# Kernel optimization log

Hardware: AMD Instinct MI355X
Metric: run time of the kernel (lower is better)

## Reference

```python
import jax, jax.numpy as jnp
import numpy as np
import math

B, T, HIDDEN = 1, 2048, 2048
N_HEADS, N_KV = 16, 8
HD = HIDDEN // N_HEADS  # 128
EPS = 1e-6
THETA = 1e6


def _rmsnorm(x, w, eps=EPS):
    return x * jax.lax.rsqrt(jnp.mean(x * x, axis=-1, keepdims=True) + eps) * w


def _rope(x, sin, cos):
    # even/odd split, non-interleaved concat output (matches get_rope)
    x1 = x[..., 0::2]
    x2 = x[..., 1::2]
    s = sin[None, :, None, :]  # [1, T, 1, HD//2]
    c = cos[None, :, None, :]
    return jnp.concatenate([x1 * c - x2 * s, x1 * s + x2 * c], axis=-1)


def setup_inputs() -> dict:
    key = jax.random.key(0)
    ks = jax.random.split(key, 6)
    x = jax.random.normal(ks[0], (B, T, HIDDEN), dtype=jnp.float32)
    Wq = 0.02 * jax.random.normal(ks[1], (HIDDEN, 2 * HIDDEN), dtype=jnp.float32)
    Wk = 0.02 * jax.random.normal(ks[2], (HIDDEN, N_KV * HD), dtype=jnp.float32)
    Wv = 0.02 * jax.random.normal(ks[3], (HIDDEN, N_KV * HD), dtype=jnp.float32)
    Wo = 0.02 * jax.random.normal(ks[4], (2 * HIDDEN, HIDDEN), dtype=jnp.float32)
    q_norm_w = jnp.ones((2 * HD,), dtype=jnp.float32)
    k_norm_w = jnp.ones((HD,), dtype=jnp.float32)
    inv_freq = 1.0 / (THETA ** (jnp.arange(0, HD, 2, dtype=jnp.float32) / HD))
    freqs = jnp.arange(T, dtype=jnp.float32)[:, None] * inv_freq[None, :]  # [T, HD//2]
    return {"x": x, "Wq": Wq, "Wk": Wk, "Wv": Wv, "Wo": Wo,
            "q_norm_w": q_norm_w, "k_norm_w": k_norm_w,
            "sin": jnp.sin(freqs), "cos": jnp.cos(freqs)}


def reference(x, Wq, Wk, Wv, Wo, q_norm_w, k_norm_w, sin, cos):
    b, t, _ = x.shape
    # projections
    q = (x @ Wq).reshape(b, t, N_HEADS, 2 * HD)
    k = (x @ Wk).reshape(b, t, N_KV, HD)
    v = (x @ Wv).reshape(b, t, N_KV, HD)
    # per-head QK RMSNorm (q_norm over 2*head_dim)
    q = _rmsnorm(q, q_norm_w)
    k = _rmsnorm(k, k_norm_w)
    # split q into 2*N_HEADS attention heads of dim HD, apply RoPE
    hq = 2 * N_HEADS
    q = _rope(q.reshape(b, t, hq, HD), sin, cos)
    k = _rope(k, sin, cos)
    # GQA: repeat kv heads
    g = hq // N_KV
    k = jnp.repeat(k, g, axis=2)  # [b, t, hq, HD]
    v = jnp.repeat(v, g, axis=2)
    # attention: no causal mask in the original module
    att = jnp.einsum('bqhd,bkhd->bhqk', q, k) / math.sqrt(HD)
    p = jax.nn.softmax(att, axis=-1)
    out = jnp.einsum('bhqk,bkhd->bqhd', p, v).reshape(b, t, hq * HD)
    return out @ Wo
```

## Files before the change

### kernel.cpp

```cpp
#include <hip/hip_runtime.h>

typedef unsigned short u16;
typedef __attribute__((ext_vector_type(8))) short bf16x8;
typedef __attribute__((ext_vector_type(4))) short s16x4;
typedef __attribute__((ext_vector_type(4))) float f32x4;

__device__ __forceinline__ float bf2f(u16 u) {
  union { unsigned u; float f; } c; c.u = ((unsigned)u) << 16; return c.f;
}
__device__ __forceinline__ u16 f2bf(float f) {
  union { float f; unsigned u; } c; c.f = f;
  return (u16)((c.u + 0x7fffu + ((c.u >> 16) & 1u)) >> 16);
}
#if __has_builtin(__builtin_amdgcn_cvt_pk_bf16_f32)
__device__ __forceinline__ unsigned pkbf(float a, float b) {
  auto v = __builtin_amdgcn_cvt_pk_bf16_f32(a, b);
  return __builtin_bit_cast(unsigned, v);
}
#else
__device__ __forceinline__ unsigned pkbf(float a, float b) {
  return (unsigned)f2bf(a) | ((unsigned)f2bf(b) << 16);
}
#endif
#if __has_builtin(__builtin_amdgcn_mfma_f32_16x16x16bf16_1k)
#define MFMA16(a, b, c) __builtin_amdgcn_mfma_f32_16x16x16bf16_1k(a, b, c, 0, 0, 0)
#define HAVE_MFMA16 1
#endif
#if __has_builtin(__builtin_amdgcn_permlane16_swap) && \
    __has_builtin(__builtin_amdgcn_permlane32_swap)
#define HAVE_PLSWAP 1
__device__ __forceinline__ void plswap32(unsigned& a, unsigned& b) {
  auto r = __builtin_amdgcn_permlane32_swap(a, b, false, false);
  a = r[0]; b = r[1];
}
__device__ __forceinline__ void plswap16(unsigned& a, unsigned& b) {
  auto r = __builtin_amdgcn_permlane16_swap(a, b, false, false);
  a = r[0]; b = r[1];
}
#endif
#if __has_builtin(__builtin_amdgcn_exp2f)
#define EXP2(x) __builtin_amdgcn_exp2f(x)
#else
#define EXP2(x) __expf((x) * 0.69314718f)
#endif
__device__ __forceinline__ void gl2lds16(const u16* g, u16* l) {
  __builtin_amdgcn_global_load_lds(
      (const __attribute__((address_space(1))) void*)g,
      (__attribute__((address_space(3))) void*)l, 16, 0, 0);
}

__device__ __forceinline__ void tr_cast_tile(const float* __restrict__ in,
                                             u16* __restrict__ out,
                                             int ldin, int ldout, int bx, int by) {
  __shared__ u16 tile[64][66];
  const int tx = threadIdx.x;
  const int lr = tx & 31, lc = tx >> 5;
  const int r0 = by << 6, c0 = bx << 6;
#pragma unroll
  for (int i = 0; i < 8; ++i) {
    int r = lc + (i << 3);
    float2 v = *(const float2*)&in[(size_t)(r0 + r) * ldin + c0 + (lr << 1)];
    *(unsigned*)&tile[r][lr << 1] = pkbf(v.x, v.y);
  }
  __syncthreads();
#pragma unroll
  for (int i = 0; i < 8; ++i) {
    int c = lc + (i << 3);
    unsigned v = (unsigned)tile[lr << 1][c] | ((unsigned)tile[(lr << 1) + 1][c] << 16);
    *(unsigned*)&out[(size_t)(c0 + c) * ldout + r0 + (lr << 1)] = v;
  }
}

__global__ __launch_bounds__(256) void prep(const float* __restrict__ x,
                                            u16* __restrict__ xb,
                                            const float* __restrict__ Wq,
                                            u16* __restrict__ WqT,
                                            const float* __restrict__ Wk,
                                            u16* __restrict__ WkT,
                                            const float* __restrict__ Wv,
                                            u16* __restrict__ WvT) {
  int b = blockIdx.x;
  if (b < 2048) {
    int i = (b * 256 + threadIdx.x) * 8;
    float4 a = *(const float4*)&x[i];
    float4 c = *(const float4*)&x[i + 4];
    union { unsigned u[4]; bf16x8 v; } w;
    w.u[0] = pkbf(a.x, a.y); w.u[1] = pkbf(a.z, a.w);
    w.u[2] = pkbf(c.x, c.y); w.u[3] = pkbf(c.z, c.w);
    *(bf16x8*)&xb[i] = w.v;
  } else if (b < 4096) {
    int t = b - 2048;
    tr_cast_tile(Wq, WqT, 4096, 2048, t & 63, t >> 6);
  } else if (b < 4608) {
    int t = b - 4096;
    tr_cast_tile(Wk, WkT, 1024, 2048, t & 15, t >> 4);
  } else {
    int t = b - 4608;
    tr_cast_tile(Wv, WvT, 1024, 2048, t & 15, t >> 4);
  }
}

__global__ __launch_bounds__(256) void transpose_cast(const float* __restrict__ in,
                                                      u16* __restrict__ out,
                                                      int ldin, int ldout) {
  tr_cast_tile(in, out, ldin, ldout, blockIdx.x, blockIdx.y);
}

__global__ __launch_bounds__(256) void gemm_bt(const u16* __restrict__ A,
                                               const u16* __restrict__ BT,
                                               u16* __restrict__ C,
                                               int M, int N, int K) {
  __shared__ u16 Asl[2][128 * 32];
  __shared__ u16 Bsl[2][128 * 32];
  const int tid = threadIdx.x;
  const int lane = tid & 63, wv = tid >> 6;
  const int lr = lane & 15, qd = lane >> 4;
  const int wr = wv >> 1, wc = wv & 1;
  const int m0 = blockIdx.y << 7, n0 = blockIdx.x << 7;
  const int srow = lane >> 2, scol = (lane & 3) << 3;
  const u16* Ag = &A[(size_t)(m0 + wv * 32 + srow) * K + scol];
  const u16* Bg = &BT[(size_t)(n0 + wv * 32 + srow) * K + scol];
  const size_t rstr16 = (size_t)16 * K;
  f32x4 acc[4][4] = {};
  for (int k0 = 0; k0 < K; k0 += 64) {
    __syncthreads();
#pragma unroll
    for (int p = 0; p < 2; ++p) {
#pragma unroll
      for (int hh = 0; hh < 2; ++hh) {
        gl2lds16(Ag + k0 + p * 32 + hh * rstr16, &Asl[p][wv * 1024 + hh * 512]);
        gl2lds16(Bg + k0 + p * 32 + hh * rstr16, &Bsl[p][wv * 1024 + hh * 512]);
      }
    }
    __syncthreads();
#pragma unroll
    for (int p = 0; p < 2; ++p) {
      bf16x8 af[4], bfr[4];
#pragma unroll
      for (int i = 0; i < 4; ++i) {
        af[i]  = *(const bf16x8*)&Asl[p][(wr * 64 + i * 16 + lr) * 32 + qd * 8];
        bfr[i] = *(const bf16x8*)&Bsl[p][(wc * 64 + i * 16 + lr) * 32 + qd * 8];
      }
#pragma unroll
      for (int mi = 0; mi < 4; ++mi)
#pragma unroll
        for (int ni = 0; ni < 4; ++ni)
          acc[mi][ni] = __builtin_amdgcn_mfma_f32_16x16x32_bf16(
              af[mi], bfr[ni], acc[mi][ni], 0, 0, 0);
    }
  }
#pragma unroll
  for (int mi = 0; mi < 4; ++mi)
#pragma unroll
    for (int ni = 0; ni < 4; ++ni)
#pragma unroll
      for (int r = 0; r < 4; ++r)
        C[(size_t)(m0 + wr * 64 + mi * 16 + qd * 4 + r) * N +
          n0 + wc * 64 + ni * 16 + lr] = f2bf(acc[mi][ni][r]);
}

__global__ __launch_bounds__(256) void gemm_bt_sk(const u16* __restrict__ A,
                                                  const u16* __restrict__ BT,
                                                  float* __restrict__ C,
                                                  int M, int N, int K, int kspan) {
  __shared__ u16 Asl[2][128 * 32];
  __shared__ u16 Bsl[2][128 * 32];
  const int tid = threadIdx.x;
  const int lane = tid & 63, wv = tid >> 6;
  const int lr = lane & 15, qd = lane >> 4;
  const int wr = wv >> 1, wc = wv & 1;
  const int m0 = blockIdx.y << 7, n0 = blockIdx.x << 7;
  const int kbeg = blockIdx.z * kspan;
  const int srow = lane >> 2, scol = (lane & 3) << 3;
  const u16* Ag = &A[(size_t)(m0 + wv * 32 + srow) * K + kbeg + scol];
  const u16* Bg = &BT[(size_t)(n0 + wv * 32 + srow) * K + kbeg + scol];
  const size_t rstr16 = (size_t)16 * K;
  f32x4 acc[4][4] = {};
  for (int k0 = 0; k0 < kspan; k0 += 64) {
    __syncthreads();
#pragma unroll
    for (int p = 0; p < 2; ++p) {
#pragma unroll
      for (int hh = 0; hh < 2; ++hh) {
        gl2lds16(Ag + k0 + p * 32 + hh * rstr16, &Asl[p][wv * 1024 + hh * 512]);
        gl2lds16(Bg + k0 + p * 32 + hh * rstr16, &Bsl[p][wv * 1024 + hh * 512]);
      }
    }
    __syncthreads();
#pragma unroll
    for (int p = 0; p < 2; ++p) {
      bf16x8 af[4], bfr[4];
#pragma unroll
      for (int i = 0; i < 4; ++i) {
        af[i]  = *(const bf16x8*)&Asl[p][(wr * 64 + i * 16 + lr) * 32 + qd * 8];
        bfr[i] = *(const bf16x8*)&Bsl[p][(wc * 64 + i * 16 + lr) * 32 + qd * 8];
      }
#pragma unroll
      for (int mi = 0; mi < 4; ++mi)
#pragma unroll
        for (int ni = 0; ni < 4; ++ni)
          acc[mi][ni] = __builtin_amdgcn_mfma_f32_16x16x32_bf16(
              af[mi], bfr[ni], acc[mi][ni], 0, 0, 0);
    }
  }
#pragma unroll
  for (int mi = 0; mi < 4; ++mi)
#pragma unroll
    for (int ni = 0; ni < 4; ++ni)
#pragma unroll
      for (int r = 0; r < 4; ++r)
        unsafeAtomicAdd(&C[(size_t)(m0 + wr * 64 + mi * 16 + qd * 4 + r) * N +
                           n0 + wc * 64 + ni * 16 + lr], acc[mi][ni][r]);
}

__global__ __launch_bounds__(256) void norm_vt(u16* __restrict__ QKV,
                                               u16* __restrict__ VTb,
                                               const float* __restrict__ qw,
                                               const float* __restrict__ kw,
                                               const float* __restrict__ sinb,
                                               const float* __restrict__ cosb) {
  int b = blockIdx.x;
  if (b >= 2048) {
    __shared__ u16 tile[64][66];
    int t = b - 2048;
    const int tx = threadIdx.x;
    const int lr = tx & 31, lc = tx >> 5;
    const int r0 = (t >> 4) << 6, c0 = (t & 15) << 6;
    const u16* in = QKV + 5120;
#pragma unroll
    for (int i = 0; i < 8; ++i) {
      int r = lc + (i << 3);
      unsigned v = *(const unsigned*)&in[(size_t)(r0 + r) * 6144 + c0 + (lr << 1)];
      *(unsigned*)&tile[r][lr << 1] = v;
    }
    __syncthreads();
#pragma unroll
    for (int i = 0; i < 8; ++i) {
      int c = lc + (i << 3);
      unsigned v = (unsigned)tile[lr << 1][c] | ((unsigned)tile[(lr << 1) + 1][c] << 16);
      *(unsigned*)&VTb[(size_t)(c0 + c) * 2048 + r0 + (lr << 1)] = v;
    }
    return;
  }
  const int t = b;
  const int wv = threadIdx.x >> 6, l = threadIdx.x & 63;
  const float sv = sinb[t * 64 + l];
  const float cv = cosb[t * 64 + l];
  const float qscale = 0.12753102543f;
  u16* Q = QKV + (size_t)t * 6144;
  u16* Kb = Q + 4096;
  for (int j = wv; j < 16; j += 4) {
    u16* base = Q + j * 256;
    float x0 = bf2f(base[2 * l]);
    float x1 = bf2f(base[2 * l + 1]);
    float x2 = bf2f(base[128 + 2 * l]);
    float x3 = bf2f(base[129 + 2 * l]);
    float ss = x0 * x0 + x1 * x1 + x2 * x2 + x3 * x3;
#pragma unroll
    for (int m = 1; m < 64; m <<= 1) ss += __shfl_xor(ss, m, 64);
    float rn = rsqrtf(ss * (1.0f / 256.0f) + 1e-6f);
    float w0 = qw[2 * l], w1 = qw[2 * l + 1];
    float w2 = qw[128 + 2 * l], w3 = qw[129 + 2 * l];
    x0 *= rn * w0; x1 *= rn * w1; x2 *= rn * w2; x3 *= rn * w3;
    base[l]       = f2bf((x0 * cv - x1 * sv) * qscale);
    base[64 + l]  = f2bf((x0 * sv + x1 * cv) * qscale);
    base[128 + l] = f2bf((x2 * cv - x3 * sv) * qscale);
    base[192 + l] = f2bf((x2 * sv + x3 * cv) * qscale);
  }
  for (int j = wv; j < 8; j += 4) {
    u16* base = Kb + j * 128;
    float x0 = bf2f(base[2 * l]);
    float x1 = bf2f(base[2 * l + 1]);
    float ss = x0 * x0 + x1 * x1;
#pragma unroll
    for (int m = 1; m < 64; m <<= 1) ss += __shfl_xor(ss, m, 64);
    float rn = rsqrtf(ss * (1.0f / 128.0f) + 1e-6f);
    float w0 = kw[2 * l], w1 = kw[2 * l + 1];
    x0 *= rn * w0; x1 *= rn * w1;
    base[l]      = f2bf(x0 * cv - x1 * sv);
    base[64 + l] = f2bf(x0 * sv + x1 * cv);
  }
}

__global__ __launch_bounds__(256, 2) void flash(const u16* __restrict__ QKV,
                                                const u16* __restrict__ VTb,
                                                u16* __restrict__ O0,
                                                u16* __restrict__ O1,
                                                float* __restrict__ L0,
                                                float* __restrict__ L1) {
  __shared__ u16 Ks0[64 * 128];
  __shared__ u16 Ks1[64 * 128];
  __shared__ u16 Vs0[128 * 64];
  __shared__ u16 Vs1[128 * 64];
  const int tid = threadIdx.x;
  const int wv = tid >> 6, lane = tid & 63;
  const int c = lane & 15, qd = lane >> 4;
  const int h = blockIdx.y, kv = h >> 2;
  const int qb = (blockIdx.x << 7) + wv * 32;
  const int z = blockIdx.z;
  u16* Ob = z ? O1 : O0;
  float* Lb = z ? L1 : L0;
  const int cx = c & 7;
  const int krow_off = lane >> 4;
  const int kpb = lane & 15;
  const int vrow_off = lane >> 3;
  const int vpb = lane & 7;
  bf16x8 qf[2][4];
#pragma unroll
  for (int ms = 0; ms < 2; ++ms)
#pragma unroll
    for (int ks = 0; ks < 4; ++ks)
      qf[ms][ks] = *(const bf16x8*)&QKV[(size_t)(qb + ms * 16 + c) * 6144 +
                                        h * 128 + ks * 32 + qd * 8];
  f32x4 o[2][8] = {};
  float lrun[2] = {0.f, 0.f};

  auto stage = [&](int k0, u16* Kd, u16* Vd) {
#pragma unroll
    for (int it = 0; it < 4; ++it) {
      int rbase = (wv * 4 + it) * 4;
      int r = rbase + krow_off;
      int klb = kpb ^ (r & 7);
      gl2lds16(&QKV[(size_t)(k0 + r) * 6144 + 4096 + kv * 128 + klb * 8],
               &Kd[rbase * 128]);
      int dbase = (wv * 4 + it) * 8;
      int d = dbase + vrow_off;
      int vlb = vpb ^ (d & 7);
      gl2lds16(&VTb[(size_t)(kv * 128 + d) * 2048 + k0 + vlb * 8],
               &Vd[dbase * 64]);
    }
  };

  auto compute = [&](const u16* Ks, const u16* Vs) {
    f32x4 s[2][4];
    __builtin_amdgcn_s_setprio(1);
#pragma unroll
    for (int ns = 0; ns < 4; ++ns) {
      f32x4 a0 = {0.f, 0.f, 0.f, 0.f}, a1 = {0.f, 0.f, 0.f, 0.f};
#pragma unroll
      for (int ks = 0; ks < 4; ++ks) {
        bf16x8 kf = *(const bf16x8*)
            &Ks[(ns * 16 + c) * 128 + (((4 * ks + qd) ^ cx) << 3)];
        a0 = __builtin_amdgcn_mfma_f32_16x16x32_bf16(kf, qf[0][ks], a0, 0, 0, 0);
        a1 = __builtin_amdgcn_mfma_f32_16x16x32_bf16(kf, qf[1][ks], a1, 0, 0, 0);
      }
      s[0][ns] = a0; s[1][ns] = a1;
    }
    __builtin_amdgcn_s_setprio(0);
#pragma unroll
    for (int ms = 0; ms < 2; ++ms) {
      float rs = 0.f;
#pragma unroll
      for (int ns = 0; ns < 4; ++ns)
#pragma unroll
        for (int r = 0; r < 4; ++r) {
          float p = EXP2(s[ms][ns][r]);
          s[ms][ns][r] = p; rs += p;
        }
      lrun[ms] += rs;
    }
#ifdef HAVE_PLSWAP
#pragma unroll
    for (int t2 = 0; t2 < 2; ++t2) {
      bf16x8 pB[2];
#pragma unroll
      for (int ms = 0; ms < 2; ++ms) {
        unsigned p0 = pkbf(s[ms][2 * t2][0],     s[ms][2 * t2][1]);
        unsigned p1 = pkbf(s[ms][2 * t2][2],     s[ms][2 * t2][3]);
        unsigned p2 = pkbf(s[ms][2 * t2 + 1][0], s[ms][2 * t2 + 1][1]);
        unsigned p3 = pkbf(s[ms][2 * t2 + 1][2], s[ms][2 * t2 + 1][3]);
        plswap32(p0, p2); plswap16(p0, p2);
        plswap32(p1, p3); plswap16(p1, p3);
        union { unsigned u[4]; bf16x8 v; } bb;
        bb.u[0] = p0; bb.u[1] = p1; bb.u[2] = p2; bb.u[3] = p3;
        pB[ms] = bb.v;
      }
      __builtin_amdgcn_s_setprio(1);
#pragma unroll
      for (int n8 = 0; n8 < 8; ++n8) {
        bf16x8 vf = *(const bf16x8*)
            &Vs[(n8 * 16 + c) * 64 + (((4 * t2 + qd) ^ cx) << 3)];
        o[0][n8] = __builtin_amdgcn_mfma_f32_16x16x32_bf16(vf, pB[0], o[0][n8], 0, 0, 0);
        o[1][n8] = __builtin_amdgcn_mfma_f32_16x16x32_bf16(vf, pB[1], o[1][n8], 0, 0, 0);
      }
      __builtin_amdgcn_s_setprio(0);
    }
#elif defined(HAVE_MFMA16)
#pragma unroll
    for (int ns = 0; ns < 4; ++ns) {
      s16x4 pb[2];
#pragma unroll
      for (int ms = 0; ms < 2; ++ms) {
        union { unsigned u[2]; s16x4 v; } pu;
        pu.u[0] = pkbf(s[ms][ns][0], s[ms][ns][1]);
        pu.u[1] = pkbf(s[ms][ns][2], s[ms][ns][3]);
        pb[ms] = pu.v;
      }
      const int voff = ((((2 * ns) + (qd >> 1)) ^ cx) << 3) + (qd & 1) * 4;
#pragma unroll
      for (int n8 = 0; n8 < 8; ++n8) {
        s16x4 vf = *(const s16x4*)&Vs[(n8 * 16 + c) * 64 + voff];
        o[0][n8] = MFMA16(vf, pb[0], o[0][n8]);
        o[1][n8] = MFMA16(vf, pb[1], o[1][n8]);
      }
    }
#else
    unsigned pk[2][4][2];
#pragma unroll
    for (int ms = 0; ms < 2; ++ms)
#pragma unroll
      for (int ns = 0; ns < 4; ++ns) {
        pk[ms][ns][0] = pkbf(s[ms][ns][0], s[ms][ns][1]);
        pk[ms][ns][1] = pkbf(s[ms][ns][2], s[ms][ns][3]);
      }
    const bool hi = lane >= 32;
    const int sl0 = ((lane >> 4) & 1) * 32 + c;
    const int sl1 = sl0 + 16;
#pragma unroll
    for (int t2 = 0; t2 < 2; ++t2) {
      union { int i[4]; bf16x8 v; } pb[2];
#pragma unroll
      for (int ms = 0; ms < 2; ++ms)
#pragma unroll
        for (int dw = 0; dw < 4; ++dw) {
          int rg = dw & 1;
          int sl = dw < 2 ? sl0 : sl1;
          int va = __shfl((int)pk[ms][2 * t2][rg], sl, 64);
          int vb = __shfl((int)pk[ms][2 * t2 + 1][rg], sl, 64);
          pb[ms].i[dw] = hi ? vb : va;
        }
#pragma unroll
      for (int n8 = 0; n8 < 8; ++n8) {
        bf16x8 vf = *(const bf16x8*)
            &Vs[(n8 * 16 + c) * 64 + (((4 * t2 + qd) ^ cx) << 3)];
        o[0][n8] = __builtin_amdgcn_mfma_f32_16x16x32_bf16(vf, pb[0].v, o[0][n8], 0, 0, 0);
        o[1][n8] = __builtin_amdgcn_mfma_f32_16x16x32_bf16(vf, pb[1].v, o[1][n8], 0, 0, 0);
      }
    }
#endif
  };

  const int kbeg = z << 10, kend = kbeg + 1024;
  stage(kbeg, Ks0, Vs0);
#pragma unroll 1
  for (int k0 = kbeg; k0 < kend; k0 += 128) {
    __syncthreads();
    stage(k0 + 64, Ks1, Vs1);
    compute(Ks0, Vs0);
    __syncthreads();
    if (k0 + 128 < kend) stage(k0 + 128, Ks0, Vs0);
    compute(Ks1, Vs1);
  }
#pragma unroll
  for (int ms = 0; ms < 2; ++ms) {
    lrun[ms] += __shfl_xor(lrun[ms], 16, 64);
    lrun[ms] += __shfl_xor(lrun[ms], 32, 64);
  }
  if (qd == 0) {
    Lb[(qb + c) * 32 + h] = lrun[0];
    Lb[(qb + 16 + c) * 32 + h] = lrun[1];
  }
#pragma unroll
  for (int ms = 0; ms < 2; ++ms)
#pragma unroll
    for (int n8 = 0; n8 < 8; ++n8) {
      union { unsigned u[2]; s16x4 v; } w;
      w.u[0] = pkbf(o[ms][n8][0], o[ms][n8][1]);
      w.u[1] = pkbf(o[ms][n8][2], o[ms][n8][3]);
      *(s16x4*)&Ob[(size_t)(qb + ms * 16 + c) * 4096 + h * 128 + n8 * 16 + qd * 4] = w.v;
    }
}

__global__ __launch_bounds__(256) void combine(u16* __restrict__ O0,
                                               const u16* __restrict__ O1,
                                               const float* __restrict__ L0,
                                               const float* __restrict__ L1) {
  int i8 = (blockIdx.x * 256 + threadIdx.x) * 8;
  int q = i8 >> 12, h = (i8 >> 7) & 31;
  float inv = 1.0f / (L0[q * 32 + h] + L1[q * 32 + h]);
  bf16x8 a = *(bf16x8*)&O0[i8];
  bf16x8 b = *(const bf16x8*)&O1[i8];
  union { unsigned u[4]; bf16x8 v; } w;
#pragma unroll
  for (int j = 0; j < 4; ++j) {
    float e0 = (bf2f((u16)a[2 * j]) + bf2f((u16)b[2 * j])) * inv;
    float e1 = (bf2f((u16)a[2 * j + 1]) + bf2f((u16)b[2 * j + 1])) * inv;
    w.u[j] = pkbf(e0, e1);
  }
  *(bf16x8*)&O0[i8] = w.v;
}

extern "C" void kernel_launch(void* const* d_in, const int* in_sizes, int n_in,
                              void* d_out, int out_size, void* d_ws, size_t ws_size,
                              hipStream_t stream) {
  const float* x    = (const float*)d_in[0];
  const float* Wq   = (const float*)d_in[1];
  const float* Wk   = (const float*)d_in[2];
  const float* Wv   = (const float*)d_in[3];
  const float* Wo   = (const float*)d_in[4];
  const float* qnw  = (const float*)d_in[5];
  const float* knw  = (const float*)d_in[6];
  const float* sinb = (const float*)d_in[7];
  const float* cosb = (const float*)d_in[8];
  float* out = (float*)d_out;
  char* ws = (char*)d_ws;
  const size_t MB = 1024 * 1024;
  u16* WqkvT = (u16*)(ws + 0 * MB);
  u16* Op0   = (u16*)(ws + 0 * MB);
  float* L0f = (float*)(ws + 16 * MB);
  float* L1f = (float*)(ws + 16 * MB + 262144);
  u16* QKV = (u16*)(ws + 24 * MB);
  u16* WoT = (u16*)(ws + 24 * MB);
  u16* xb  = (u16*)(ws + 48 * MB);
  u16* Op1 = (u16*)(ws + 48 * MB);
  u16* VTb = (u16*)(ws + 64 * MB);

  prep<<<5120, 256, 0, stream>>>(x, xb, Wq, WqkvT,
                                 Wk, WqkvT + (size_t)4096 * 2048,
                                 Wv, WqkvT + (size_t)5120 * 2048);
  gemm_bt<<<dim3(48, 16), 256, 0, stream>>>(xb, WqkvT, QKV, 2048, 6144, 2048);
  norm_vt<<<2560, 256, 0, stream>>>(QKV, VTb, qnw, knw, sinb, cosb);
  flash<<<dim3(16, 32, 2), 256, 0, stream>>>(QKV, VTb, Op0, Op1, L0f, L1f);
  transpose_cast<<<dim3(32, 64), 256, 0, stream>>>(Wo, WoT, 2048, 4096);
  combine<<<4096, 256, 0, stream>>>(Op0, Op1, L0f, L1f);
  hipMemsetAsync(out, 0, (size_t)2048 * 2048 * 4, stream);
  gemm_bt_sk<<<dim3(16, 16, 2), 256, 0, stream>>>(Op0, WoT, out, 2048, 2048, 4096, 2048);
  (void)in_sizes; (void)n_in; (void)out_size; (void)ws_size;
}
```

Baseline: 383.4 us.

## Enlarge flash query tile to 64 rows per wave and remap grid by KV group

Each wave now processes 64 query rows instead of 32, so every K/V fragment read from LDS feeds four MFMAs rather than two, and the block covers 256 queries. The grid becomes 1D with 512 blocks, ordered so consecutive blocks share a KV head and key-split half, which is meant to improve L2 reuse of K/V. The compute loop is restructured to interleave QK and PV per 32-key half to limit live score registers. The cost is much higher register pressure (o accumulators double to 128 floats) under launch_bounds(256,2), which risks spills or lower occupancy, and half as many blocks are launched.

New measurement: 733.7 us. 1.91x slower.

```diff
diff --git a/kernel.cpp b/kernel.cpp
--- a/kernel.cpp
+++ b/kernel.cpp
@@ -295,9 +295,11 @@
   const int tid = threadIdx.x;
   const int wv = tid >> 6, lane = tid & 63;
   const int c = lane & 15, qd = lane >> 4;
-  const int h = blockIdx.y, kv = h >> 2;
-  const int qb = (blockIdx.x << 7) + wv * 32;
-  const int z = blockIdx.z;
+  const int s_ = blockIdx.x;
+  const int g = s_ & 15, i_ = s_ >> 4;
+  const int kv = g >> 1, z = g & 1;
+  const int h = kv * 4 + (i_ >> 3);
+  const int qb = ((i_ & 7) << 8) + wv * 64;
   u16* Ob = z ? O1 : O0;
   float* Lb = z ? L1 : L0;
   const int cx = c & 7;
@@ -305,15 +307,15 @@
   const int kpb = lane & 15;
   const int vrow_off = lane >> 3;
   const int vpb = lane & 7;
-  bf16x8 qf[2][4];
-#pragma unroll
-  for (int ms = 0; ms < 2; ++ms)
+  bf16x8 qf[4][4];
+#pragma unroll
+  for (int ms = 0; ms < 4; ++ms)
 #pragma unroll
     for (int ks = 0; ks < 4; ++ks)
       qf[ms][ks] = *(const bf16x8*)&QKV[(size_t)(qb + ms * 16 + c) * 6144 +
                                         h * 128 + ks * 32 + qd * 8];
-  f32x4 o[2][8] = {};
-  float lrun[2] = {0.f, 0.f};
+  f32x4 o[4][8] = {};
+  float lrun[4] = {0.f, 0.f, 0.f, 0.f};
 
   auto stage = [&](int k0, u16* Kd, u16* Vd) {
 #pragma unroll
@@ -332,43 +334,49 @@
   };
 
   auto compute = [&](const u16* Ks, const u16* Vs) {
-    f32x4 s[2][4];
-    __builtin_amdgcn_s_setprio(1);
-#pragma unroll
-    for (int ns = 0; ns < 4; ++ns) {
-      f32x4 a0 = {0.f, 0.f, 0.f, 0.f}, a1 = {0.f, 0.f, 0.f, 0.f};
-#pragma unroll
-      for (int ks = 0; ks < 4; ++ks) {
-        bf16x8 kf = *(const bf16x8*)
-            &Ks[(ns * 16 + c) * 128 + (((4 * ks + qd) ^ cx) << 3)];
-        a0 = __builtin_amdgcn_mfma_f32_16x16x32_bf16(kf, qf[0][ks], a0, 0, 0, 0);
-        a1 = __builtin_amdgcn_mfma_f32_16x16x32_bf16(kf, qf[1][ks], a1, 0, 0, 0);
-      }
-      s[0][ns] = a0; s[1][ns] = a1;
-    }
-    __builtin_amdgcn_s_setprio(0);
-#pragma unroll
-    for (int ms = 0; ms < 2; ++ms) {
-      float rs = 0.f;
-#pragma unroll
-      for (int ns = 0; ns < 4; ++ns)
-#pragma unroll
-        for (int r = 0; r < 4; ++r) {
-          float p = EXP2(s[ms][ns][r]);
-          s[ms][ns][r] = p; rs += p;
+#pragma unroll
+    for (int t2 = 0; t2 < 2; ++t2) {
+      f32x4 s[4][2];
+      __builtin_amdgcn_s_setprio(1);
+#pragma unroll
+      for (int j = 0; j < 2; ++j) {
+        int ns = 2 * t2 + j;
+        f32x4 a[4];
+#pragma unroll
+        for (int ms = 0; ms < 4; ++ms) a[ms] = f32x4{0.f, 0.f, 0.f, 0.f};
+#pragma unroll
+        for (int ks = 0; ks < 4; ++ks) {
+          bf16x8 kf = *(const bf16x8*)
+              &Ks[(ns * 16 + c) * 128 + (((4 * ks + qd) ^ cx) << 3)];
+#pragma unroll
+          for (int ms = 0; ms < 4; ++ms)
+            a[ms] = __builtin_amdgcn_mfma_f32_16x16x32_bf16(kf, qf[ms][ks],
+                                                            a[ms], 0, 0, 0);
         }
-      lrun[ms] += rs;
-    }
+#pragma unroll
+        for (int ms = 0; ms < 4; ++ms) s[ms][j] = a[ms];
+      }
+      __builtin_amdgcn_s_setprio(0);
+#pragma unroll
+      for (int ms = 0; ms < 4; ++ms) {
+        float rs = 0.f;
+#pragma unroll
+        for (int j = 0; j < 2; ++j)
+#pragma unroll
+          for (int r = 0; r < 4; ++r) {
+            float p = EXP2(s[ms][j][r]);
+            s[ms][j][r] = p; rs += p;
+          }
+        lrun[ms] += rs;
+      }
 #ifdef HAVE_PLSWAP
-#pragma unroll
-    for (int t2 = 0; t2 < 2; ++t2) {
-      bf16x8 pB[2];
-#pragma unroll
-      for (int ms = 0; ms < 2; ++ms) {
-        unsigned p0 = pkbf(s[ms][2 * t2][0],     s[ms][2 * t2][1]);
-        unsigned p1 = pkbf(s[ms][2 * t2][2],     s[ms][2 * t2][3]);
-        unsigned p2 = pkbf(s[ms][2 * t2 + 1][0], s[ms][2 * t2 + 1][1]);
-        unsigned p3 = pkbf(s[ms][2 * t2 + 1][2], s[ms][2 * t2 + 1][3]);
+      bf16x8 pB[4];
+#pragma unroll
+      for (int ms = 0; ms < 4; ++ms) {
+        unsigned p0 = pkbf(s[ms][0][0], s[ms][0][1]);
+        unsigned p1 = pkbf(s[ms][0][2], s[ms][0][3]);
+        unsigned p2 = pkbf(s[ms][1][0], s[ms][1][1]);
+        unsigned p3 = pkbf(s[ms][1][2], s[ms][1][3]);
         plswap32(p0, p2); plswap16(p0, p2);
         plswap32(p1, p3); plswap16(p1, p3);
         union { unsigned u[4]; bf16x8 v; } bb;
@@ -380,64 +388,35 @@
       for (int n8 = 0; n8 < 8; ++n8) {
         bf16x8 vf = *(const bf16x8*)
             &Vs[(n8 * 16 + c) * 64 + (((4 * t2 + qd) ^ cx) << 3)];
-        o[0][n8] = __builtin_amdgcn_mfma_f32_16x16x32_bf16(vf, pB[0], o[0][n8], 0, 0, 0);
-        o[1][n8] = __builtin_amdgcn_mfma_f32_16x16x32_bf16(vf, pB[1], o[1][n8], 0, 0, 0);
+#pragma unroll
+        for (int ms = 0; ms < 4; ++ms)
+          o[ms][n8] = __builtin_amdgcn_mfma_f32_16x16x32_bf16(vf, pB[ms],
+                                                              o[ms][n8], 0, 0, 0);
       }
       __builtin_amdgcn_s_setprio(0);
-    }
 #elif defined(HAVE_MFMA16)
 #pragma unroll
-    for (int ns = 0; ns < 4; ++ns) {
-      s16x4 pb[2];
-#pragma unroll
-      for (int ms = 0; ms < 2; ++ms) {
-        union { unsigned u[2]; s16x4 v; } pu;
-        pu.u[0] = pkbf(s[ms][ns][0], s[ms][ns][1]);
-        pu.u[1] = pkbf(s[ms][ns][2], s[ms][ns][3]);
-        pb[ms] = pu.v;
-      }
-      const int voff = ((((2 * ns) + (qd >> 1)) ^ cx) << 3) + (qd & 1) * 4;
-#pragma unroll
-      for (int n8 = 0; n8 < 8; ++n8) {
-        s16x4 vf = *(const s16x4*)&Vs[(n8 * 16 + c) * 64 + voff];
-        o[0][n8] = MFMA16(vf, pb[0], o[0][n8]);
-        o[1][n8] = MFMA16(vf, pb[1], o[1][n8]);
-      }
-    }
-#else
-    unsigned pk[2][4][2];
-#pragma unroll
-    for (int ms = 0; ms < 2; ++ms)
-#pragma unroll
-      for (int ns = 0; ns < 4; ++ns) {
-        pk[ms][ns][0] = pkbf(s[ms][ns][0], s[ms][ns][1]);
-        pk[ms][ns][1] = pkbf(s[ms][ns][2], s[ms][ns][3]);
-      }
-    const bool hi = lane >= 32;
-    const int sl0 = ((lane >> 4) & 1) * 32 + c;
-    const int sl1 = sl0 + 16;
-#pragma unroll
-    for (int t2 = 0; t2 < 2; ++t2) {
-      union { int i[4]; bf16x8 v; } pb[2];
-#pragma unroll
-      for (int ms = 0; ms < 2; ++ms)
-#pragma unroll
-        for (int dw = 0; dw < 4; ++dw) {
-          int rg = dw & 1;
-          int sl = dw < 2 ? sl0 : sl1;
-          int va = __shfl((int)pk[ms][2 * t2][rg], sl, 64);
-          int vb = __shfl((int)pk[ms][2 * t2 + 1][rg], sl, 64);
-          pb[ms].i[dw] = hi ? vb : va;
+      for (int j = 0; j < 2; ++j) {
+        int ns = 2 * t2 + j;
+        s16x4 pb[4];
+#pragma unroll
+        for (int ms = 0; ms < 4; ++ms) {
+          union { unsigned u[2]; s16x4 v; } pu;
+          pu.u[0] = pkbf(s[ms][j][0], s[ms][j][1]);
+          pu.u[1] = pkbf(s[ms][j][2], s[ms][j][3]);
+          pb[ms] = pu.v;
         }
-#pragma unroll
-      for (int n8 = 0; n8 < 8; ++n8) {
-        bf16x8 vf = *(const bf16x8*)
-            &Vs[(n8 * 16 + c) * 64 + (((4 * t2 + qd) ^ cx) << 3)];
-        o[0][n8] = __builtin_amdgcn_mfma_f32_16x16x32_bf16(vf, pb[0].v, o[0][n8], 0, 0, 0);
-        o[1][n8] = __builtin_amdgcn_mfma_f32_16x16x32_bf16(vf, pb[1].v, o[1][n8], 0, 0, 0);
-      }
-    }
+        const int voff = ((((2 * ns) + (qd >> 1)) ^ cx) << 3) + (qd & 1) * 4;
+#pragma unroll
+        for (int n8 = 0; n8 < 8; ++n8) {
+          s16x4 vf = *(const s16x4*)&Vs[(n8 * 16 + c) * 64 + voff];
+#pragma unroll
+          for (int ms = 0; ms < 4; ++ms)
+            o[ms][n8] = MFMA16(vf, pb[ms], o[ms][n8]);
+        }
+      }
 #endif
+    }
   };
 
   const int kbeg = z << 10, kend = kbeg + 1024;
@@ -452,16 +431,17 @@
     compute(Ks1, Vs1);
   }
 #pragma unroll
-  for (int ms = 0; ms < 2; ++ms) {
+  for (int ms = 0; ms < 4; ++ms) {
     lrun[ms] += __shfl_xor(lrun[ms], 16, 64);
     lrun[ms] += __shfl_xor(lrun[ms], 32, 64);
   }
   if (qd == 0) {
-    Lb[(qb + c) * 32 + h] = lrun[0];
-    Lb[(qb + 16 + c) * 32 + h] = lrun[1];
-  }
-#pragma unroll
-  for (int ms = 0; ms < 2; ++ms)
+#pragma unroll
+    for (int ms = 0; ms < 4; ++ms)
+      Lb[(qb + ms * 16 + c) * 32 + h] = lrun[ms];
+  }
+#pragma unroll
+  for (int ms = 0; ms < 4; ++ms)
 #pragma unroll
     for (int n8 = 0; n8 < 8; ++n8) {
       union { unsigned u[2]; s16x4 v; } w;
@@ -520,7 +500,7 @@
                                  Wv, WqkvT + (size_t)5120 * 2048);
   gemm_bt<<<dim3(48, 16), 256, 0, stream>>>(xb, WqkvT, QKV, 2048, 6144, 2048);
   norm_vt<<<2560, 256, 0, stream>>>(QKV, VTb, qnw, knw, sinb, cosb);
-  flash<<<dim3(16, 32, 2), 256, 0, stream>>>(QKV, VTb, Op0, Op1, L0f, L1f);
+  flash<<<512, 256, 0, stream>>>(QKV, VTb, Op0, Op1, L0f, L1f);
   transpose_cast<<<dim3(32, 64), 256, 0, stream>>>(Wo, WoT, 2048, 4096);
   combine<<<4096, 256, 0, stream>>>(Op0, Op1, L0f, L1f);
   hipMemsetAsync(out, 0, (size_t)2048 * 2048 * 4, stream);
```

## Drop flash split-KV and remap workgroups so heads sharing KV co-run

Applied to the files above, without the earlier changes.

Removes the two-way key split in the flash attention kernel, so each workgroup now loops over all 2048 keys and writes a single partial output and row sum. The combine kernel reads one buffer instead of two. A 1D grid with a swizzled block index spreads consecutive workgroups across 8 heads (one per XCD, assuming round-robin dispatch), so blocks that share KV data can land on the same XCD's L2. The intent is to cut the extra partial-output traffic and combine work. The cost is halving the number of workgroups to 512, which may lower occupancy and tail balance on the 256-CU part.

After: 369.5 us. -3.6%, faster.

```diff
diff --git a/kernel.cpp b/kernel.cpp
--- a/kernel.cpp
+++ b/kernel.cpp
@@ -284,10 +284,8 @@
 
 __global__ __launch_bounds__(256, 2) void flash(const u16* __restrict__ QKV,
                                                 const u16* __restrict__ VTb,
-                                                u16* __restrict__ O0,
-                                                u16* __restrict__ O1,
-                                                float* __restrict__ L0,
-                                                float* __restrict__ L1) {
+                                                u16* __restrict__ O,
+                                                float* __restrict__ L) {
   __shared__ u16 Ks0[64 * 128];
   __shared__ u16 Ks1[64 * 128];
   __shared__ u16 Vs0[128 * 64];
@@ -295,11 +293,12 @@
   const int tid = threadIdx.x;
   const int wv = tid >> 6, lane = tid & 63;
   const int c = lane & 15, qd = lane >> 4;
-  const int h = blockIdx.y, kv = h >> 2;
-  const int qb = (blockIdx.x << 7) + wv * 32;
-  const int z = blockIdx.z;
-  u16* Ob = z ? O1 : O0;
-  float* Lb = z ? L1 : L0;
+  const int wgid = blockIdx.x;
+  const int r8 = wgid & 7, t_ = wgid >> 3;
+  const int qx = t_ & 15, hh = t_ >> 4;
+  const int h = r8 + (hh << 3);
+  const int kv = h >> 2;
+  const int qb = (qx << 7) + wv * 32;
   const int cx = c & 7;
   const int krow_off = lane >> 4;
   const int kpb = lane & 15;
@@ -440,15 +439,14 @@
 #endif
   };
 
-  const int kbeg = z << 10, kend = kbeg + 1024;
-  stage(kbeg, Ks0, Vs0);
+  stage(0, Ks0, Vs0);
 #pragma unroll 1
-  for (int k0 = kbeg; k0 < kend; k0 += 128) {
+  for (int k0 = 0; k0 < 2048; k0 += 128) {
     __syncthreads();
     stage(k0 + 64, Ks1, Vs1);
     compute(Ks0, Vs0);
     __syncthreads();
-    if (k0 + 128 < kend) stage(k0 + 128, Ks0, Vs0);
+    if (k0 + 128 < 2048) stage(k0 + 128, Ks0, Vs0);
     compute(Ks1, Vs1);
   }
 #pragma unroll
@@ -457,8 +455,8 @@
     lrun[ms] += __shfl_xor(lrun[ms], 32, 64);
   }
   if (qd == 0) {
-    Lb[(qb + c) * 32 + h] = lrun[0];
-    Lb[(qb + 16 + c) * 32 + h] = lrun[1];
+    L[(qb + c) * 32 + h] = lrun[0];
+    L[(qb + 16 + c) * 32 + h] = lrun[1];
   }
 #pragma unroll
   for (int ms = 0; ms < 2; ++ms)
@@ -467,27 +465,24 @@
       union { unsigned u[2]; s16x4 v; } w;
       w.u[0] = pkbf(o[ms][n8][0], o[ms][n8][1]);
       w.u[1] = pkbf(o[ms][n8][2], o[ms][n8][3]);
-      *(s16x4*)&Ob[(size_t)(qb + ms * 16 + c) * 4096 + h * 128 + n8 * 16 + qd * 4] = w.v;
-    }
-}
-
-__global__ __launch_bounds__(256) void combine(u16* __restrict__ O0,
-                                               const u16* __restrict__ O1,
-                                               const float* __restrict__ L0,
-                                               const float* __restrict__ L1) {
+      *(s16x4*)&O[(size_t)(qb + ms * 16 + c) * 4096 + h * 128 + n8 * 16 + qd * 4] = w.v;
+    }
+}
+
+__global__ __launch_bounds__(256) void combine(u16* __restrict__ O,
+                                               const float* __restrict__ L) {
   int i8 = (blockIdx.x * 256 + threadIdx.x) * 8;
   int q = i8 >> 12, h = (i8 >> 7) & 31;
-  float inv = 1.0f / (L0[q * 32 + h] + L1[q * 32 + h]);
-  bf16x8 a = *(bf16x8*)&O0[i8];
-  bf16x8 b = *(const bf16x8*)&O1[i8];
+  float inv = 1.0f / L[q * 32 + h];
+  bf16x8 a = *(bf16x8*)&O[i8];
   union { unsigned u[4]; bf16x8 v; } w;
 #pragma unroll
   for (int j = 0; j < 4; ++j) {
-    float e0 = (bf2f((u16)a[2 * j]) + bf2f((u16)b[2 * j])) * inv;
-    float e1 = (bf2f((u16)a[2 * j + 1]) + bf2f((u16)b[2 * j + 1])) * inv;
+    float e0 = bf2f((u16)a[2 * j]) * inv;
+    float e1 = bf2f((u16)a[2 * j + 1]) * inv;
     w.u[j] = pkbf(e0, e1);
   }
-  *(bf16x8*)&O0[i8] = w.v;
+  *(bf16x8*)&O[i8] = w.v;
 }
 
 extern "C" void kernel_launch(void* const* d_in, const int* in_sizes, int n_in,
@@ -508,11 +503,9 @@
   u16* WqkvT = (u16*)(ws + 0 * MB);
   u16* Op0   = (u16*)(ws + 0 * MB);
   float* L0f = (float*)(ws + 16 * MB);
-  float* L1f = (float*)(ws + 16 * MB + 262144);
   u16* QKV = (u16*)(ws + 24 * MB);
   u16* WoT = (u16*)(ws + 24 * MB);
   u16* xb  = (u16*)(ws + 48 * MB);
-  u16* Op1 = (u16*)(ws + 48 * MB);
   u16* VTb = (u16*)(ws + 64 * MB);
 
   prep<<<5120, 256, 0, stream>>>(x, xb, Wq, WqkvT,
@@ -520,9 +513,9 @@
                                  Wv, WqkvT + (size_t)5120 * 2048);
   gemm_bt<<<dim3(48, 16), 256, 0, stream>>>(xb, WqkvT, QKV, 2048, 6144, 2048);
   norm_vt<<<2560, 256, 0, stream>>>(QKV, VTb, qnw, knw, sinb, cosb);
-  flash<<<dim3(16, 32, 2), 256, 0, stream>>>(QKV, VTb, Op0, Op1, L0f, L1f);
+  flash<<<512, 256, 0, stream>>>(QKV, VTb, Op0, L0f);
   transpose_cast<<<dim3(32, 64), 256, 0, stream>>>(Wo, WoT, 2048, 4096);
-  combine<<<4096, 256, 0, stream>>>(Op0, Op1, L0f, L1f);
+  combine<<<4096, 256, 0, stream>>>(Op0, L0f);
   hipMemsetAsync(out, 0, (size_t)2048 * 2048 * 4, stream);
   gemm_bt_sk<<<dim3(16, 16, 2), 256, 0, stream>>>(Op0, WoT, out, 2048, 2048, 4096, 2048);
   (void)in_sizes; (void)n_in; (void)out_size; (void)ws_size;
```
